# Kernel optimization log

Measured on AMD Instinct MI355X. Metric: run time of the kernel, lower is better.

## Reference

```python
import jax, jax.numpy as jnp
import numpy as np

B, S, INPUT_DIM = 16, 2048, 768
G, V = 2, 320            # num_codebooks, codebook_size
D = INPUT_DIM // G       # codebook_dim = 384
OUT_DIM = 768
TEMP = 1.0
EPS = 1e-10


def setup_inputs() -> dict:
    key = jax.random.key(0)
    ks = jax.random.split(key, 7)
    z = jax.random.normal(ks[0], (B, S, INPUT_DIM), dtype=jnp.float32)
    noise = jax.random.uniform(ks[1], (B, S, G, V), dtype=jnp.float32)
    # logits_projection: Linear(codebook_dim -> codebook_size)
    W_logits = jax.random.normal(ks[2], (D, V), dtype=jnp.float32) / np.sqrt(D)
    b_logits = jnp.zeros((V,), dtype=jnp.float32)
    codebooks = jax.random.normal(ks[3], (G, V, D), dtype=jnp.float32)
    # output_projection: Linear(input_dim -> output_dim)
    W_out = jax.random.normal(ks[4], (INPUT_DIM, OUT_DIM), dtype=jnp.float32) / np.sqrt(INPUT_DIM)
    b_out = jnp.zeros((OUT_DIM,), dtype=jnp.float32)
    return {"z": z, "noise": noise, "W_logits": W_logits, "b_logits": b_logits,
            "codebooks": codebooks, "W_out": W_out, "b_out": b_out}


def reference(z, noise, W_logits, b_logits, codebooks, W_out, b_out):
    b, s, _ = z.shape
    g, v, d = codebooks.shape
    zr = z.reshape(b, s, g, d)                                   # [B,S,G,D]
    logits = jnp.einsum('bsgd,dv->bsgv', zr, W_logits) + b_logits
    # training-mode gumbel noise
    gumbel = -jnp.log(-jnp.log(noise + EPS) + EPS)
    logits = (logits + gumbel) / TEMP
    probs = jax.nn.softmax(logits, axis=-1)                      # [B,S,G,V]
    indices = jnp.argmax(probs, axis=-1)                         # [B,S,G]
    hard = jax.nn.one_hot(indices, v, dtype=probs.dtype)
    quantized = hard - jax.lax.stop_gradient(probs) + probs      # straight-through
    quantized = jnp.einsum('bsgv,gvd->bsgd', quantized, codebooks)
    quantized = quantized.reshape(b, s, g * d)
    return quantized @ W_out + b_out
```

## Files before the change

kernel.cpp:

```cpp
#include <hip/hip_runtime.h>
#include <math.h>

#define BS_TOT 32768
#define IN_DIM 768
#define G_N 2
#define V_N 320
#define D_N 384
#define OUT_N 768
#define EPS_F 1e-10f

typedef _Float16 f16x8 __attribute__((ext_vector_type(8)));
typedef float    f32x16 __attribute__((ext_vector_type(16)));

#define GLOBAL_LOAD_LDS16(gaddr, laddr)                                        \
  __builtin_amdgcn_global_load_lds(                                            \
      (const __attribute__((address_space(1))) unsigned int*)(gaddr),          \
      (__attribute__((address_space(3))) unsigned int*)(laddr), 16, 0, 0)

__global__ __launch_bounds__(256) void prep_w(
    const float* __restrict__ Wl, _Float16* __restrict__ Wp)
{
    int e = blockIdx.x * 256 + threadIdx.x;
    if (e >= D_N * V_N) return;
    int k = e / V_N, v = e - k * V_N;
    int c = v >> 6, col = v & 63;
    int t = k >> 4, kh = (k >> 3) & 1, j = k & 7;
    float w = Wl[e];
    _Float16 a = (_Float16)w;
    float r = (w - (float)a) * 4096.f;
    size_t u0 = (size_t)c * 6144 + ((t * 2 + 0) * 2 + kh) * 64 + col;
    size_t u1 = (size_t)c * 6144 + ((t * 2 + 1) * 2 + kh) * 64 + col;
    Wp[u0 * 8 + j] = a;
    Wp[u1 * 8 + j] = (_Float16)r;
}

__global__ __launch_bounds__(256) void precompute_P(
    const float* __restrict__ cb, const float* __restrict__ Wo,
    float* __restrict__ P)
{
    const int tid = threadIdx.x;
    const int c0  = blockIdx.x * 256;
    const int r0  = blockIdx.y * 8;
    const int g   = r0 / V_N;
    __shared__ float As[8][D_N];
    {
        const float4* src = (const float4*)(cb + (size_t)r0 * D_N);
        float4* dst = (float4*)(&As[0][0]);
        #pragma unroll
        for (int p = 0; p < 3; ++p) dst[tid + p * 256] = src[tid + p * 256];
    }
    __syncthreads();
    float acc[8];
    #pragma unroll
    for (int i = 0; i < 8; ++i) acc[i] = 0.f;
    const float* wp = Wo + ((size_t)g * D_N) * OUT_N + c0 + tid;
    for (int d = 0; d < D_N; d += 4) {
        float w0 = wp[(size_t)(d + 0) * OUT_N];
        float w1 = wp[(size_t)(d + 1) * OUT_N];
        float w2 = wp[(size_t)(d + 2) * OUT_N];
        float w3 = wp[(size_t)(d + 3) * OUT_N];
        #pragma unroll
        for (int i = 0; i < 8; ++i) {
            float4 a = *(const float4*)&As[i][d];
            acc[i] = fmaf(a.x, w0, acc[i]);
            acc[i] = fmaf(a.y, w1, acc[i]);
            acc[i] = fmaf(a.z, w2, acc[i]);
            acc[i] = fmaf(a.w, w3, acc[i]);
        }
    }
    #pragma unroll
    for (int i = 0; i < 8; ++i)
        P[(size_t)(r0 + i) * OUT_N + c0 + tid] = acc[i];
}

__global__ __launch_bounds__(512, 4) void logits_part(
    const float* __restrict__ z, const float* __restrict__ noise,
    const f16x8* __restrict__ Wp, const float* __restrict__ bl,
    float* __restrict__ pv, int* __restrict__ pi)
{
    const int tid = threadIdx.x;
    const int ln  = tid & 63;
    const int wv  = tid >> 6;
    const int lh  = ln >> 5;
    const int l5  = ln & 31;
    const int cg  = blockIdx.x;
    const int cc  = cg % 5;
    const int g   = cg / 5;
    const int m0  = blockIdx.y * 256;

    __shared__ f16x8 Bs[3072];

    const f16x8* wsrc = Wp + (size_t)cc * 6144;

#define STAGEQ(Q, SLOT)                                                        \
    {                                                                          \
        _Pragma("unroll")                                                      \
        for (int i_ = 0; i_ < 3; ++i_)                                         \
            GLOBAL_LOAD_LDS16(wsrc + (Q) * 1536 + i_ * 512 + wv * 64 + ln,     \
                              Bs + (SLOT) * 1536 + i_ * 512 + wv * 64);        \
    }

    STAGEQ(0, 0)
    STAGEQ(1, 1)

    const float* zb = z + (size_t)(m0 + wv * 32 + l5) * IN_DIM + g * D_N + lh * 8;
    float4 pa0 = *(const float4*)(zb);
    float4 pa1 = *(const float4*)(zb + 4);
    float4 pb0 = *(const float4*)(zb + 16);
    float4 pb1 = *(const float4*)(zb + 20);

    f32x16 aM0, aM1, aC0, aC1;
    #pragma unroll
    for (int i = 0; i < 16; ++i) { aM0[i] = 0.f; aM1[i] = 0.f; aC0[i] = 0.f; aC1[i] = 0.f; }

    __syncthreads();

#define STEP(T, SLOT, P0, P1)                                                  \
    {                                                                          \
        float x_[8] = {P0.x, P0.y, P0.z, P0.w, P1.x, P1.y, P1.z, P1.w};        \
        f16x8 h1, h2;                                                          \
        _Pragma("unroll")                                                      \
        for (int i_ = 0; i_ < 8; ++i_) {                                       \
            _Float16 a_ = (_Float16)x_[i_];                                    \
            h1[i_] = a_;                                                       \
            h2[i_] = (_Float16)((x_[i_] - (float)a_) * 4096.f);                \
        }                                                                      \
        if ((T) + 2 < 24) {                                                    \
            P0 = *(const float4*)(zb + ((T) + 2) * 16);                        \
            P1 = *(const float4*)(zb + ((T) + 2) * 16 + 4);                    \
        }                                                                      \
        const int tq2_ = ((T) % 6) * 2;                                        \
        f16x8 Bm0 = Bs[(SLOT) * 1536 + ((tq2_ + 0) * 2 + lh) * 64 + l5];       \
        f16x8 Bc0 = Bs[(SLOT) * 1536 + ((tq2_ + 1) * 2 + lh) * 64 + l5];       \
        f16x8 Bm1 = Bs[(SLOT) * 1536 + ((tq2_ + 0) * 2 + lh) * 64 + 32 + l5];  \
        f16x8 Bc1 = Bs[(SLOT) * 1536 + ((tq2_ + 1) * 2 + lh) * 64 + 32 + l5];  \
        aM0 = __builtin_amdgcn_mfma_f32_32x32x16_f16(h1, Bm0, aM0, 0, 0, 0);   \
        aC0 = __builtin_amdgcn_mfma_f32_32x32x16_f16(h1, Bc0, aC0, 0, 0, 0);   \
        aC0 = __builtin_amdgcn_mfma_f32_32x32x16_f16(h2, Bm0, aC0, 0, 0, 0);   \
        aM1 = __builtin_amdgcn_mfma_f32_32x32x16_f16(h1, Bm1, aM1, 0, 0, 0);   \
        aC1 = __builtin_amdgcn_mfma_f32_32x32x16_f16(h1, Bc1, aC1, 0, 0, 0);   \
        aC1 = __builtin_amdgcn_mfma_f32_32x32x16_f16(h2, Bm1, aC1, 0, 0, 0);   \
    }

    STEP(0, 0, pa0, pa1) STEP(1, 0, pb0, pb1) STEP(2, 0, pa0, pa1)
    STEP(3, 0, pb0, pb1) STEP(4, 0, pa0, pa1) STEP(5, 0, pb0, pb1)
    __syncthreads();
    STAGEQ(2, 0)
    STEP(6, 1, pa0, pa1) STEP(7, 1, pb0, pb1) STEP(8, 1, pa0, pa1)
    STEP(9, 1, pb0, pb1) STEP(10, 1, pa0, pa1) STEP(11, 1, pb0, pb1)
    __syncthreads();
    STAGEQ(3, 1)
    STEP(12, 0, pa0, pa1) STEP(13, 0, pb0, pb1) STEP(14, 0, pa0, pa1)
    STEP(15, 0, pb0, pb1) STEP(16, 0, pa0, pa1) STEP(17, 0, pb0, pb1)
    __syncthreads();
    STEP(18, 1, pa0, pa1) STEP(19, 1, pb0, pb1) STEP(20, 1, pa0, pa1)
    STEP(21, 1, pb0, pb1) STEP(22, 1, pa0, pa1) STEP(23, 1, pb0, pb1)

#undef STEP
#undef STAGEQ

    const float blv0 = bl[cc * 64 + l5];
    const float blv1 = bl[cc * 64 + 32 + l5];
    const int   col0 = cc * 64 + l5;
    const int   col1 = cc * 64 + 32 + l5;

    #pragma unroll
    for (int r = 0; r < 16; ++r) {
        const int rowloc = (r & 3) + 8 * (r >> 2) + 4 * lh;
        const int grow   = m0 + wv * 32 + rowloc;
        const float* np_ = noise + ((size_t)grow * G_N + g) * V_N + cc * 64 + l5;
        float u0 = np_[0];
        float u1 = np_[32];
        float g0 = -__logf(-__logf(u0 + EPS_F) + EPS_F);
        float g1 = -__logf(-__logf(u1 + EPS_F) + EPS_F);
        float v0 = aM0[r] + 2.44140625e-4f * aC0[r] + blv0 + g0;
        float v1 = aM1[r] + 2.44140625e-4f * aC1[r] + blv1 + g1;
        float best = v0; int bi = col0;
        if (v1 > best) { best = v1; bi = col1; }
        #pragma unroll
        for (int off = 1; off < 32; off <<= 1) {
            float ov = __shfl_xor(best, off);
            int   oi = __shfl_xor(bi, off);
            if (ov > best || (ov == best && oi < bi)) { best = ov; bi = oi; }
        }
        if (l5 == 0) {
            pv[(size_t)(g * 5 + cc) * BS_TOT + grow] = best;
            pi[(size_t)(g * 5 + cc) * BS_TOT + grow] = bi;
        }
    }
}

__global__ __launch_bounds__(256) void finish_gather(
    const float* __restrict__ P, const float* __restrict__ pv,
    const int* __restrict__ pi, const float* __restrict__ bo,
    float* __restrict__ out)
{
    const int tid  = threadIdx.x;
    const int row0 = blockIdx.x << 2;
    __shared__ int sI[2][4];
    if (tid < 8) {
        const int gg  = tid >> 2, rl = tid & 3;
        const int row = row0 + rl;
        const float* pvb = pv + (size_t)gg * 5 * BS_TOT + row;
        const int*   pib = pi + (size_t)gg * 5 * BS_TOT + row;
        float best = pvb[0];
        int   bi   = pib[0];
        #pragma unroll
        for (int c = 1; c < 5; ++c) {
            float v = pvb[(size_t)c * BS_TOT];
            int   i = pib[(size_t)c * BS_TOT];
            if (v > best) { best = v; bi = i; }
        }
        sI[gg][rl] = bi;
    }
    __syncthreads();
    const float4* Pv  = (const float4*)P;
    const float4* bov = (const float4*)bo;
    #pragma unroll
    for (int p = 0; p < 3; ++p) {
        int f   = tid + (p << 8);
        int rl  = f / 192;
        int c4  = f - rl * 192;
        int i0  = sI[0][rl];
        int i1  = sI[1][rl];
        float4 a  = Pv[(size_t)i0 * 192 + c4];
        float4 b2 = Pv[(size_t)(V_N + i1) * 192 + c4];
        float4 c  = bov[c4];
        float4 r;
        r.x = a.x + b2.x + c.x;
        r.y = a.y + b2.y + c.y;
        r.z = a.z + b2.z + c.z;
        r.w = a.w + b2.w + c.w;
        ((float4*)(out + (size_t)(row0 + rl) * OUT_N))[c4] = r;
    }
}

extern "C" void kernel_launch(void* const* d_in, const int* in_sizes, int n_in,
                              void* d_out, int out_size, void* d_ws, size_t ws_size,
                              hipStream_t stream)
{
    const float* z     = (const float*)d_in[0];
    const float* noise = (const float*)d_in[1];
    const float* Wl    = (const float*)d_in[2];
    const float* bl    = (const float*)d_in[3];
    const float* cb    = (const float*)d_in[4];
    const float* Wo    = (const float*)d_in[5];
    const float* bo    = (const float*)d_in[6];
    float* out = (float*)d_out;

    float*     P  = (float*)d_ws;
    float*     pv = (float*)((char*)d_ws + 1966080);
    int*       pi = (int*)((char*)d_ws + 3276800);
    _Float16*  Wp = (_Float16*)((char*)d_ws + 4587520);

    prep_w<<<(D_N * V_N + 255) / 256, 256, 0, stream>>>(Wl, Wp);

    dim3 gA(OUT_N / 256, (G_N * V_N) / 8);
    precompute_P<<<gA, 256, 0, stream>>>(cb, Wo, P);

    dim3 gB(10, BS_TOT / 256);
    logits_part<<<gB, 512, 0, stream>>>(z, noise, (const f16x8*)Wp, bl, pv, pi);

    finish_gather<<<BS_TOT / 4, 256, 0, stream>>>(P, pv, pi, bo, out);
}
```

Before: 368.1 us.

## Fuse gather into logits kernel via last-block atomic counter and XCD-aware tile mapping

The separate finish_gather kernel is removed. The last of the 10 logits blocks to finish a 256-row tile, detected through an atomic counter that prep_w zeroes, now reduces the partial argmaxes and writes the gathered P rows plus bias. The grid is flattened to 1D and remapped so that all 10 blocks of a row tile land on the same XCD (j&7), which keeps z and pv reuse in that XCD's L2. This saves one kernel launch and a pass over pv/pi, but the tail work of 256 rows x 768 outputs now runs on only one block per tile, which can serialise at the end of the kernel.

```diff
diff --git a/kernel.cpp b/kernel.cpp
--- a/kernel.cpp
+++ b/kernel.cpp
@@ -18,8 +18,10 @@
       (__attribute__((address_space(3))) unsigned int*)(laddr), 16, 0, 0)
 
 __global__ __launch_bounds__(256) void prep_w(
-    const float* __restrict__ Wl, _Float16* __restrict__ Wp)
-{
+    const float* __restrict__ Wl, _Float16* __restrict__ Wp,
+    int* __restrict__ ctr)
+{
+    if (blockIdx.x == 0 && threadIdx.x < 128) ctr[threadIdx.x] = 0;
     int e = blockIdx.x * 256 + threadIdx.x;
     if (e >= D_N * V_N) return;
     int k = e / V_N, v = e - k * V_N;
@@ -76,17 +78,24 @@
 __global__ __launch_bounds__(512, 4) void logits_part(
     const float* __restrict__ z, const float* __restrict__ noise,
     const f16x8* __restrict__ Wp, const float* __restrict__ bl,
-    float* __restrict__ pv, int* __restrict__ pi)
+    float* __restrict__ pv, int* __restrict__ pi,
+    int* __restrict__ ctr, const float* __restrict__ P,
+    const float* __restrict__ bo, float* __restrict__ out)
 {
     const int tid = threadIdx.x;
     const int ln  = tid & 63;
     const int wv  = tid >> 6;
     const int lh  = ln >> 5;
     const int l5  = ln & 31;
-    const int cg  = blockIdx.x;
-    const int cc  = cg % 5;
-    const int g   = cg / 5;
-    const int m0  = blockIdx.y * 256;
+    const int j    = blockIdx.x;
+    const int xcd  = j & 7;
+    const int slot = j >> 3;
+    const int mtq  = slot / 10;
+    const int sub  = slot - mtq * 10;
+    const int mt   = mtq * 8 + xcd;
+    const int cc   = sub % 5;
+    const int g    = sub / 5;
+    const int m0   = mt * 256;
 
     __shared__ f16x8 Bs[3072];
 
@@ -188,21 +197,20 @@
             pi[(size_t)(g * 5 + cc) * BS_TOT + grow] = bi;
         }
     }
-}
-
-__global__ __launch_bounds__(256) void finish_gather(
-    const float* __restrict__ P, const float* __restrict__ pv,
-    const int* __restrict__ pi, const float* __restrict__ bo,
-    float* __restrict__ out)
-{
-    const int tid  = threadIdx.x;
-    const int row0 = blockIdx.x << 2;
-    __shared__ int sI[2][4];
-    if (tid < 8) {
-        const int gg  = tid >> 2, rl = tid & 3;
-        const int row = row0 + rl;
-        const float* pvb = pv + (size_t)gg * 5 * BS_TOT + row;
-        const int*   pib = pi + (size_t)gg * 5 * BS_TOT + row;
+
+    __threadfence();
+    __syncthreads();
+    int* sW   = (int*)&Bs[0];
+    if (tid == 0) sW[512] = (atomicAdd(&ctr[mt], 1) == 9) ? 1 : 0;
+    __syncthreads();
+    if (sW[512] == 0) return;
+    __threadfence();
+
+    {
+        const int row = tid >> 1;
+        const int gg  = tid & 1;
+        const float* pvb = pv + (size_t)gg * 5 * BS_TOT + (m0 + row);
+        const int*   pib = pi + (size_t)gg * 5 * BS_TOT + (m0 + row);
         float best = pvb[0];
         int   bi   = pib[0];
         #pragma unroll
@@ -211,27 +219,30 @@
             int   i = pib[(size_t)c * BS_TOT];
             if (v > best) { best = v; bi = i; }
         }
-        sI[gg][rl] = bi;
-    }
-    __syncthreads();
-    const float4* Pv  = (const float4*)P;
-    const float4* bov = (const float4*)bo;
-    #pragma unroll
-    for (int p = 0; p < 3; ++p) {
-        int f   = tid + (p << 8);
-        int rl  = f / 192;
-        int c4  = f - rl * 192;
-        int i0  = sI[0][rl];
-        int i1  = sI[1][rl];
-        float4 a  = Pv[(size_t)i0 * 192 + c4];
-        float4 b2 = Pv[(size_t)(V_N + i1) * 192 + c4];
-        float4 c  = bov[c4];
-        float4 r;
-        r.x = a.x + b2.x + c.x;
-        r.y = a.y + b2.y + c.y;
-        r.z = a.z + b2.z + c.z;
-        r.w = a.w + b2.w + c.w;
-        ((float4*)(out + (size_t)(row0 + rl) * OUT_N))[c4] = r;
+        sW[gg * 256 + row] = bi;
+    }
+    __syncthreads();
+
+    {
+        const float4* Pv  = (const float4*)P;
+        const float4* bov = (const float4*)bo;
+        #pragma unroll 4
+        for (int p = 0; p < 96; ++p) {
+            int f  = p * 512 + tid;
+            int rl = f / 192;
+            int c4 = f - rl * 192;
+            int i0 = sW[rl];
+            int i1 = sW[256 + rl];
+            float4 a  = Pv[(size_t)i0 * 192 + c4];
+            float4 b2 = Pv[(size_t)(V_N + i1) * 192 + c4];
+            float4 c  = bov[c4];
+            float4 r;
+            r.x = a.x + b2.x + c.x;
+            r.y = a.y + b2.y + c.y;
+            r.z = a.z + b2.z + c.z;
+            r.w = a.w + b2.w + c.w;
+            ((float4*)(out + (size_t)(m0 + rl) * OUT_N))[c4] = r;
+        }
     }
 }
 
@@ -248,18 +259,17 @@
     const float* bo    = (const float*)d_in[6];
     float* out = (float*)d_out;
 
-    float*     P  = (float*)d_ws;
-    float*     pv = (float*)((char*)d_ws + 1966080);
-    int*       pi = (int*)((char*)d_ws + 3276800);
-    _Float16*  Wp = (_Float16*)((char*)d_ws + 4587520);
-
-    prep_w<<<(D_N * V_N + 255) / 256, 256, 0, stream>>>(Wl, Wp);
+    float*     P   = (float*)d_ws;
+    float*     pv  = (float*)((char*)d_ws + 1966080);
+    int*       pi  = (int*)((char*)d_ws + 3276800);
+    _Float16*  Wp  = (_Float16*)((char*)d_ws + 4587520);
+    int*       ctr = (int*)((char*)d_ws + 5079040);
+
+    prep_w<<<(D_N * V_N + 255) / 256, 256, 0, stream>>>(Wl, Wp, ctr);
 
     dim3 gA(OUT_N / 256, (G_N * V_N) / 8);
     precompute_P<<<gA, 256, 0, stream>>>(cb, Wo, P);
 
-    dim3 gB(10, BS_TOT / 256);
-    logits_part<<<gB, 512, 0, stream>>>(z, noise, (const f16x8*)Wp, bl, pv, pi);
-
-    finish_gather<<<BS_TOT / 4, 256, 0, stream>>>(P, pv, pi, bo, out);
-}
+    logits_part<<<1280, 512, 0, stream>>>(
+        z, noise, (const f16x8*)Wp, bl, pv, pi, ctr, P, bo, out);
+}
```

Result: slower. 845.4 us (+129.7%).

## Pre-split z into fp16 hi/lo and remap blocks for XCD-local L2 reuse

Applied to the files above, without the earlier changes.

Adds a prep kernel that converts z into fp16 high/low split pairs once, so the logits kernel loads ready-made MFMA operands instead of converting per block. The logits grid is flattened and remapped so all column-group blocks for the same row tile run on the same XCD, improving L2 reuse of z rows. The prep pass adds an extra full read and write of z-sized data and needs a large workspace. It falls back to the old path when the workspace is too small.

```diff
diff --git a/kernel.cpp b/kernel.cpp
--- a/kernel.cpp
+++ b/kernel.cpp
@@ -32,6 +32,25 @@
     size_t u1 = (size_t)c * 6144 + ((t * 2 + 1) * 2 + kh) * 64 + col;
     Wp[u0 * 8 + j] = a;
     Wp[u1 * 8 + j] = (_Float16)r;
+}
+
+__global__ __launch_bounds__(256) void prep_z(
+    const float* __restrict__ z, f16x8* __restrict__ zsp)
+{
+    int e = blockIdx.x * 256 + threadIdx.x;
+    const float4* src = (const float4*)z;
+    float4 q0 = src[(size_t)e * 2];
+    float4 q1 = src[(size_t)e * 2 + 1];
+    float x[8] = {q0.x, q0.y, q0.z, q0.w, q1.x, q1.y, q1.z, q1.w};
+    f16x8 h1, h2;
+    #pragma unroll
+    for (int i = 0; i < 8; ++i) {
+        _Float16 a = (_Float16)x[i];
+        h1[i] = a;
+        h2[i] = (_Float16)((x[i] - (float)a) * 4096.f);
+    }
+    zsp[(size_t)e * 2]     = h1;
+    zsp[(size_t)e * 2 + 1] = h2;
 }
 
 __global__ __launch_bounds__(256) void precompute_P(
@@ -73,20 +92,26 @@
         P[(size_t)(r0 + i) * OUT_N + c0 + tid] = acc[i];
 }
 
+template<int ZSP>
 __global__ __launch_bounds__(512, 4) void logits_part(
-    const float* __restrict__ z, const float* __restrict__ noise,
-    const f16x8* __restrict__ Wp, const float* __restrict__ bl,
-    float* __restrict__ pv, int* __restrict__ pi)
+    const float* __restrict__ z, const f16x8* __restrict__ zsp,
+    const float* __restrict__ noise, const f16x8* __restrict__ Wp,
+    const float* __restrict__ bl, float* __restrict__ pv, int* __restrict__ pi)
 {
     const int tid = threadIdx.x;
     const int ln  = tid & 63;
     const int wv  = tid >> 6;
     const int lh  = ln >> 5;
     const int l5  = ln & 31;
-    const int cg  = blockIdx.x;
-    const int cc  = cg % 5;
-    const int g   = cg / 5;
-    const int m0  = blockIdx.y * 256;
+    const int j    = blockIdx.x;
+    const int xcd  = j & 7;
+    const int slot = j >> 3;
+    const int mtq  = slot / 10;
+    const int sub  = slot - mtq * 10;
+    const int mt   = mtq * 8 + xcd;
+    const int cc   = sub % 5;
+    const int g    = sub / 5;
+    const int m0   = mt * 256;
 
     __shared__ f16x8 Bs[3072];
 
@@ -103,11 +128,20 @@
     STAGEQ(0, 0)
     STAGEQ(1, 1)
 
-    const float* zb = z + (size_t)(m0 + wv * 32 + l5) * IN_DIM + g * D_N + lh * 8;
-    float4 pa0 = *(const float4*)(zb);
-    float4 pa1 = *(const float4*)(zb + 4);
-    float4 pb0 = *(const float4*)(zb + 16);
-    float4 pb1 = *(const float4*)(zb + 20);
+    const float* zb   = z + (size_t)(m0 + wv * 32 + l5) * IN_DIM + g * D_N + lh * 8;
+    const f16x8* zrow = zsp + ((size_t)(m0 + wv * 32 + l5) * 96 + g * 48 + lh) * 2;
+
+    f16x8  paH = {}, paL = {}, pbH = {}, pbL = {};
+    float4 fa0 = {}, fa1 = {}, fb0 = {}, fb1 = {};
+    if (ZSP) {
+        paH = zrow[0]; paL = zrow[1];
+        pbH = zrow[4]; pbL = zrow[5];
+    } else {
+        fa0 = *(const float4*)(zb);
+        fa1 = *(const float4*)(zb + 4);
+        fb0 = *(const float4*)(zb + 16);
+        fb1 = *(const float4*)(zb + 20);
+    }
 
     f32x16 aM0, aM1, aC0, aC1;
     #pragma unroll
@@ -115,19 +149,27 @@
 
     __syncthreads();
 
-#define STEP(T, SLOT, P0, P1)                                                  \
+#define STEP(T, SLOT, PH, PL, F0, F1)                                          \
     {                                                                          \
-        float x_[8] = {P0.x, P0.y, P0.z, P0.w, P1.x, P1.y, P1.z, P1.w};        \
         f16x8 h1, h2;                                                          \
-        _Pragma("unroll")                                                      \
-        for (int i_ = 0; i_ < 8; ++i_) {                                       \
-            _Float16 a_ = (_Float16)x_[i_];                                    \
-            h1[i_] = a_;                                                       \
-            h2[i_] = (_Float16)((x_[i_] - (float)a_) * 4096.f);                \
-        }                                                                      \
-        if ((T) + 2 < 24) {                                                    \
-            P0 = *(const float4*)(zb + ((T) + 2) * 16);                        \
-            P1 = *(const float4*)(zb + ((T) + 2) * 16 + 4);                    \
+        if (ZSP) {                                                             \
+            h1 = PH; h2 = PL;                                                  \
+            if ((T) + 2 < 24) {                                                \
+                PH = zrow[((T) + 2) * 4];                                      \
+                PL = zrow[((T) + 2) * 4 + 1];                                  \
+            }                                                                  \
+        } else {                                                               \
+            float x_[8] = {F0.x, F0.y, F0.z, F0.w, F1.x, F1.y, F1.z, F1.w};    \
+            _Pragma("unroll")                                                  \
+            for (int i_ = 0; i_ < 8; ++i_) {                                   \
+                _Float16 a_ = (_Float16)x_[i_];                                \
+                h1[i_] = a_;                                                   \
+                h2[i_] = (_Float16)((x_[i_] - (float)a_) * 4096.f);            \
+            }                                                                  \
+            if ((T) + 2 < 24) {                                                \
+                F0 = *(const float4*)(zb + ((T) + 2) * 16);                    \
+                F1 = *(const float4*)(zb + ((T) + 2) * 16 + 4);                \
+            }                                                                  \
         }                                                                      \
         const int tq2_ = ((T) % 6) * 2;                                        \
         f16x8 Bm0 = Bs[(SLOT) * 1536 + ((tq2_ + 0) * 2 + lh) * 64 + l5];       \
@@ -142,19 +184,23 @@
         aC1 = __builtin_amdgcn_mfma_f32_32x32x16_f16(h2, Bm1, aC1, 0, 0, 0);   \
     }
 
-    STEP(0, 0, pa0, pa1) STEP(1, 0, pb0, pb1) STEP(2, 0, pa0, pa1)
-    STEP(3, 0, pb0, pb1) STEP(4, 0, pa0, pa1) STEP(5, 0, pb0, pb1)
+    STEP(0, 0, paH, paL, fa0, fa1) STEP(1, 0, pbH, pbL, fb0, fb1)
+    STEP(2, 0, paH, paL, fa0, fa1) STEP(3, 0, pbH, pbL, fb0, fb1)
+    STEP(4, 0, paH, paL, fa0, fa1) STEP(5, 0, pbH, pbL, fb0, fb1)
     __syncthreads();
     STAGEQ(2, 0)
-    STEP(6, 1, pa0, pa1) STEP(7, 1, pb0, pb1) STEP(8, 1, pa0, pa1)
-    STEP(9, 1, pb0, pb1) STEP(10, 1, pa0, pa1) STEP(11, 1, pb0, pb1)
+    STEP(6, 1, paH, paL, fa0, fa1) STEP(7, 1, pbH, pbL, fb0, fb1)
+    STEP(8, 1, paH, paL, fa0, fa1) STEP(9, 1, pbH, pbL, fb0, fb1)
+    STEP(10, 1, paH, paL, fa0, fa1) STEP(11, 1, pbH, pbL, fb0, fb1)
     __syncthreads();
     STAGEQ(3, 1)
-    STEP(12, 0, pa0, pa1) STEP(13, 0, pb0, pb1) STEP(14, 0, pa0, pa1)
-    STEP(15, 0, pb0, pb1) STEP(16, 0, pa0, pa1) STEP(17, 0, pb0, pb1)
-    __syncthreads();
-    STEP(18, 1, pa0, pa1) STEP(19, 1, pb0, pb1) STEP(20, 1, pa0, pa1)
-    STEP(21, 1, pb0, pb1) STEP(22, 1, pa0, pa1) STEP(23, 1, pb0, pb1)
+    STEP(12, 0, paH, paL, fa0, fa1) STEP(13, 0, pbH, pbL, fb0, fb1)
+    STEP(14, 0, paH, paL, fa0, fa1) STEP(15, 0, pbH, pbL, fb0, fb1)
+    STEP(16, 0, paH, paL, fa0, fa1) STEP(17, 0, pbH, pbL, fb0, fb1)
+    __syncthreads();
+    STEP(18, 1, paH, paL, fa0, fa1) STEP(19, 1, pbH, pbL, fb0, fb1)
+    STEP(20, 1, paH, paL, fa0, fa1) STEP(21, 1, pbH, pbL, fb0, fb1)
+    STEP(22, 1, paH, paL, fa0, fa1) STEP(23, 1, pbH, pbL, fb0, fb1)
 
 #undef STEP
 #undef STAGEQ
@@ -248,18 +294,26 @@
     const float* bo    = (const float*)d_in[6];
     float* out = (float*)d_out;
 
-    float*     P  = (float*)d_ws;
-    float*     pv = (float*)((char*)d_ws + 1966080);
-    int*       pi = (int*)((char*)d_ws + 3276800);
-    _Float16*  Wp = (_Float16*)((char*)d_ws + 4587520);
+    float*     P   = (float*)d_ws;
+    float*     pv  = (float*)((char*)d_ws + 1966080);
+    int*       pi  = (int*)((char*)d_ws + 3276800);
+    _Float16*  Wp  = (_Float16*)((char*)d_ws + 4587520);
+    f16x8*     zsp = (f16x8*)((char*)d_ws + 5079040);
+    const bool use_zsp = ws_size >= (size_t)5079040 + 100663296ull;
 
     prep_w<<<(D_N * V_N + 255) / 256, 256, 0, stream>>>(Wl, Wp);
 
     dim3 gA(OUT_N / 256, (G_N * V_N) / 8);
     precompute_P<<<gA, 256, 0, stream>>>(cb, Wo, P);
 
-    dim3 gB(10, BS_TOT / 256);
-    logits_part<<<gB, 512, 0, stream>>>(z, noise, (const f16x8*)Wp, bl, pv, pi);
+    if (use_zsp) {
+        prep_z<<<(BS_TOT * 96) / 256, 256, 0, stream>>>(z, zsp);
+        logits_part<1><<<1280, 512, 0, stream>>>(
+            z, zsp, noise, (const f16x8*)Wp, bl, pv, pi);
+    } else {
+        logits_part<0><<<1280, 512, 0, stream>>>(
+            z, zsp, noise, (const f16x8*)Wp, bl, pv, pi);
+    }
 
     finish_gather<<<BS_TOT / 4, 256, 0, stream>>>(P, pv, pi, bo, out);
 }
```

New measurement: 391.8 us. 1.06x slower.
